# Optimization experiments

Measured on AMD Instinct MI355X. Metric: run time of the kernel, lower is better.

Reference implementation:

```python
import jax, jax.numpy as jnp
import numpy as np

K0 = 16                       # probe slice length (hard-coded in kernel)
TAU = 2.053748910631823       # t-test threshold (|tau| of kernel constant)


def setup_inputs() -> dict:
    key = jax.random.key(0)
    k1, k2, k3 = jax.random.split(key, 3)
    B, DIN, DOUT = 8192, 4096, 4096
    x = jax.random.normal(k1, (B, DIN), dtype=jnp.float32)
    W = jax.random.normal(k2, (DOUT, DIN), dtype=jnp.float32)
    bias = jax.random.normal(k3, (DOUT,), dtype=jnp.float32)
    return {"x": x, "W": W, "bias": bias}


def reference(x, W, bias):
    # --- partial dot over the first K0 columns of K (the probe) ---
    x0 = x[:, :K0]                    # [B, K0]
    w0 = W[:, :K0]                    # [DOUT, K0]
    y1 = x0 @ w0.T                    # [B, DOUT]  sum_k x_k * w_k
    # sum of squared elementwise products: prod_k^2 = x_k^2 * w_k^2
    s2 = (x0 * x0) @ (w0 * w0).T      # [B, DOUT]
    # --- per-(row, column) t-statistic and early-exit decision ---
    tstat = jnp.abs(y1) / jnp.sqrt(s2 / K0)
    passed = tstat < TAU              # True -> column deemed insignificant, zeroed
    # --- full linear (active columns keep full accumulation + bias) ---
    full = x @ W.T + bias[None, :]    # [B, DOUT]
    return jnp.where(passed, 0.0, full)
```

## Files before the change

kernel.cpp:

```cpp
#include <hip/hip_runtime.h>
#include <cstdint>
#include <cstddef>

#define TAU_D 2.053748910631823
#define M_DIM 8192
#define N_DIM 4096
#define K_DIM 4096
#define NIT   32

typedef float f32x4  __attribute__((ext_vector_type(4)));
typedef short bf16x8 __attribute__((ext_vector_type(8)));

typedef __attribute__((address_space(1))) void gvoid_t;
typedef __attribute__((address_space(3))) void lvoid_t;

__device__ __forceinline__ void gload_lds16(const void* g, void* l) {
    __builtin_amdgcn_global_load_lds((const gvoid_t*)g, (lvoid_t*)l, 16, 0, 0);
}

__device__ __forceinline__ unsigned int pack2bf(float lo, float hi) {
    unsigned int ul = __float_as_uint(lo);
    unsigned int uh = __float_as_uint(hi);
    ul = (ul + 0x7FFFu + ((ul >> 16) & 1u)) >> 16;
    uh = (uh + 0x7FFFu + ((uh >> 16) & 1u)) >> 16;
    return ul | (uh << 16);
}

__global__ void cvt_f32_to_bf16(const float4* __restrict__ in,
                                uint2* __restrict__ out, int n4) {
    int i = blockIdx.x * blockDim.x + threadIdx.x;
    const int stride = gridDim.x * blockDim.x;
    for (; i < n4; i += stride) {
        float4 a = in[i];
        uint2 o;
        o.x = pack2bf(a.x, a.y);
        o.y = pack2bf(a.z, a.w);
        out[i] = o;
    }
}

#define BARRIER() do { __builtin_amdgcn_s_barrier(); \
                       __builtin_amdgcn_sched_barrier(0); } while (0)

__global__ __launch_bounds__(512, 2) void gemm_masked8(
    const unsigned short* __restrict__ Ab,
    const unsigned short* __restrict__ Bb,
    const float* __restrict__ X,
    const float* __restrict__ Wt,
    const float* __restrict__ bias,
    float* __restrict__ out)
{
    __shared__ __align__(16) char lds[131072];

    const int tid  = threadIdx.x;
    const int wave = tid >> 6;
    const int lane = tid & 63;
    const int lr = lane & 15;
    const int lq = lane >> 4;
    const int wm = wave >> 2;
    const int wn = wave & 3;

    const int flat = blockIdx.x;
    const int xcd  = flat & 7;
    const int s    = flat >> 3;
    const int rnd  = s >> 5;
    const int jj   = s & 31;
    const int trow = rnd * 16 + ((xcd >> 2) << 3) + (jj >> 2);
    const int tcol = ((xcd & 3) << 2) + (jj & 3);
    const int rowBase = trow * 256;
    const int colBase = tcol * 256;

    f32x4 acc[8][4];
    #pragma unroll
    for (int i = 0; i < 8; ++i)
        #pragma unroll
        for (int n = 0; n < 4; ++n)
            acc[i][n] = (f32x4){0.f, 0.f, 0.f, 0.f};

    const int srow  = tid >> 3;
    const int sslot = (tid & 7) ^ (srow & 7);
    const unsigned short* aSrc =
        Ab + (size_t)(rowBase + srow) * K_DIM + sslot * 8;
    const unsigned short* bSrc =
        Bb + (size_t)(colBase + srow) * K_DIM + sslot * 8;

    const unsigned R0A = 0, R0B = 32768, R1A = 65536, R1B = 98304;

    auto stageA = [&](int kst, unsigned reg) {
        #pragma unroll
        for (int i = 0; i < 4; ++i)
            gload_lds16(aSrc + (size_t)i * 64 * K_DIM + kst * 64,
                        lds + reg + i * 8192 + wave * 1024);
    };
    auto stageB = [&](int kst, unsigned reg) {
        #pragma unroll
        for (int i = 0; i < 4; ++i)
            gload_lds16(bSrc + (size_t)i * 64 * K_DIM + kst * 64,
                        lds + reg + i * 8192 + wave * 1024);
    };

    const unsigned kk0 = (unsigned)((lq) ^ (lr & 7)) * 16;
    const unsigned kk1 = (unsigned)((4 + lq) ^ (lr & 7)) * 16;
    const unsigned rowA = (unsigned)(wm * 128 + lr) * 128;
    const unsigned rowB = (unsigned)(wn * 64 + lr) * 128;

    stageA(0, R0A);
    stageB(0, R0B);
    stageA(1, R1A);
    asm volatile("s_waitcnt vmcnt(4)" ::: "memory");
    BARRIER();

    bf16x8 aF[4][2];
    bf16x8 bF0[2][2];
    bf16x8 bF1[2][2];

    for (int j = 0; j < NIT; ++j) {
        const int ka = 2 * j;
        const int kb = 2 * j + 1;
        const bool stg = (j + 1 < NIT);

        #pragma unroll
        for (int m = 0; m < 4; ++m) {
            aF[m][0] = *(const bf16x8*)(lds + R0A + rowA + m * 2048 + kk0);
            aF[m][1] = *(const bf16x8*)(lds + R0A + rowA + m * 2048 + kk1);
        }
        #pragma unroll
        for (int n = 0; n < 2; ++n) {
            bF0[n][0] = *(const bf16x8*)(lds + R0B + rowB + n * 2048 + kk0);
            bF0[n][1] = *(const bf16x8*)(lds + R0B + rowB + n * 2048 + kk1);
        }
        stageB(kb, R1B);
        BARRIER();
        __builtin_amdgcn_s_setprio(1);
        #pragma unroll
        for (int m = 0; m < 4; ++m)
            #pragma unroll
            for (int n = 0; n < 2; ++n)
                #pragma unroll
                for (int ks = 0; ks < 2; ++ks)
                    acc[m][n] = __builtin_amdgcn_mfma_f32_16x16x32_bf16(
                        aF[m][ks], bF0[n][ks], acc[m][n], 0, 0, 0);
        __builtin_amdgcn_s_setprio(0);
        BARRIER();

        #pragma unroll
        for (int n = 0; n < 2; ++n) {
            bF1[n][0] = *(const bf16x8*)(lds + R0B + rowB + (2 + n) * 2048 + kk0);
            bF1[n][1] = *(const bf16x8*)(lds + R0B + rowB + (2 + n) * 2048 + kk1);
        }
        BARRIER();
        __builtin_amdgcn_s_setprio(1);
        #pragma unroll
        for (int m = 0; m < 4; ++m)
            #pragma unroll
            for (int n = 0; n < 2; ++n)
                #pragma unroll
                for (int ks = 0; ks < 2; ++ks)
                    acc[m][2 + n] = __builtin_amdgcn_mfma_f32_16x16x32_bf16(
                        aF[m][ks], bF1[n][ks], acc[m][2 + n], 0, 0, 0);
        __builtin_amdgcn_s_setprio(0);
        BARRIER();

        #pragma unroll
        for (int m = 0; m < 4; ++m) {
            aF[m][0] = *(const bf16x8*)(lds + R0A + rowA + (4 + m) * 2048 + kk0);
            aF[m][1] = *(const bf16x8*)(lds + R0A + rowA + (4 + m) * 2048 + kk1);
        }
        BARRIER();
        __builtin_amdgcn_s_setprio(1);
        #pragma unroll
        for (int m = 0; m < 4; ++m)
            #pragma unroll
            for (int n = 0; n < 2; ++n)
                #pragma unroll
                for (int ks = 0; ks < 2; ++ks)
                    acc[4 + m][2 + n] = __builtin_amdgcn_mfma_f32_16x16x32_bf16(
                        aF[m][ks], bF1[n][ks], acc[4 + m][2 + n], 0, 0, 0);
        __builtin_amdgcn_s_setprio(0);
        BARRIER();

        if (stg) stageA(ka + 2, R0A);
        BARRIER();
        __builtin_amdgcn_s_setprio(1);
        #pragma unroll
        for (int m = 0; m < 4; ++m)
            #pragma unroll
            for (int n = 0; n < 2; ++n)
                #pragma unroll
                for (int ks = 0; ks < 2; ++ks)
                    acc[4 + m][n] = __builtin_amdgcn_mfma_f32_16x16x32_bf16(
                        aF[m][ks], bF0[n][ks], acc[4 + m][n], 0, 0, 0);
        __builtin_amdgcn_s_setprio(0);
        if (stg) {
            asm volatile("s_waitcnt vmcnt(4)" ::: "memory");
        } else {
            asm volatile("s_waitcnt vmcnt(0)" ::: "memory");
        }
        BARRIER();

        #pragma unroll
        for (int m = 0; m < 4; ++m) {
            aF[m][0] = *(const bf16x8*)(lds + R1A + rowA + m * 2048 + kk0);
            aF[m][1] = *(const bf16x8*)(lds + R1A + rowA + m * 2048 + kk1);
        }
        #pragma unroll
        for (int n = 0; n < 2; ++n) {
            bF0[n][0] = *(const bf16x8*)(lds + R1B + rowB + n * 2048 + kk0);
            bF0[n][1] = *(const bf16x8*)(lds + R1B + rowB + n * 2048 + kk1);
        }
        if (stg) stageB(ka + 2, R0B);
        BARRIER();
        __builtin_amdgcn_s_setprio(1);
        #pragma unroll
        for (int m = 0; m < 4; ++m)
            #pragma unroll
            for (int n = 0; n < 2; ++n)
                #pragma unroll
                for (int ks = 0; ks < 2; ++ks)
                    acc[m][n] = __builtin_amdgcn_mfma_f32_16x16x32_bf16(
                        aF[m][ks], bF0[n][ks], acc[m][n], 0, 0, 0);
        __builtin_amdgcn_s_setprio(0);
        BARRIER();

        #pragma unroll
        for (int n = 0; n < 2; ++n) {
            bF1[n][0] = *(const bf16x8*)(lds + R1B + rowB + (2 + n) * 2048 + kk0);
            bF1[n][1] = *(const bf16x8*)(lds + R1B + rowB + (2 + n) * 2048 + kk1);
        }
        BARRIER();
        __builtin_amdgcn_s_setprio(1);
        #pragma unroll
        for (int m = 0; m < 4; ++m)
            #pragma unroll
            for (int n = 0; n < 2; ++n)
                #pragma unroll
                for (int ks = 0; ks < 2; ++ks)
                    acc[m][2 + n] = __builtin_amdgcn_mfma_f32_16x16x32_bf16(
                        aF[m][ks], bF1[n][ks], acc[m][2 + n], 0, 0, 0);
        __builtin_amdgcn_s_setprio(0);
        BARRIER();

        #pragma unroll
        for (int m = 0; m < 4; ++m) {
            aF[m][0] = *(const bf16x8*)(lds + R1A + rowA + (4 + m) * 2048 + kk0);
            aF[m][1] = *(const bf16x8*)(lds + R1A + rowA + (4 + m) * 2048 + kk1);
        }
        BARRIER();
        __builtin_amdgcn_s_setprio(1);
        #pragma unroll
        for (int m = 0; m < 4; ++m)
            #pragma unroll
            for (int n = 0; n < 2; ++n)
                #pragma unroll
                for (int ks = 0; ks < 2; ++ks)
                    acc[4 + m][2 + n] = __builtin_amdgcn_mfma_f32_16x16x32_bf16(
                        aF[m][ks], bF1[n][ks], acc[4 + m][2 + n], 0, 0, 0);
        __builtin_amdgcn_s_setprio(0);
        BARRIER();

        if (stg) stageA(kb + 2, R1A);
        BARRIER();
        __builtin_amdgcn_s_setprio(1);
        #pragma unroll
        for (int m = 0; m < 4; ++m)
            #pragma unroll
            for (int n = 0; n < 2; ++n)
                #pragma unroll
                for (int ks = 0; ks < 2; ++ks)
                    acc[4 + m][n] = __builtin_amdgcn_mfma_f32_16x16x32_bf16(
                        aF[m][ks], bF0[n][ks], acc[4 + m][n], 0, 0, 0);
        __builtin_amdgcn_s_setprio(0);
        asm volatile("s_waitcnt vmcnt(4)" ::: "memory");
        BARRIER();
    }

    __syncthreads();
    float* x0s = (float*)(lds);
    float* w0s = (float*)(lds + 16384);
    #pragma unroll
    for (int i = 0; i < 2; ++i) {
        int idx = tid + i * 512;
        int r = idx >> 2, qq = (idx & 3) << 2;
        *(f32x4*)(x0s + r * 16 + qq) =
            *(const f32x4*)(X + (size_t)(rowBase + r) * K_DIM + qq);
        *(f32x4*)(w0s + r * 16 + qq) =
            *(const f32x4*)(Wt + (size_t)(colBase + r) * K_DIM + qq);
    }
    __syncthreads();

    const float TAU32 = (float)TAU_D;

    #pragma unroll
    for (int np = 0; np < 4; np += 2) {
        float wv[2][16];
        float bv[2];
        #pragma unroll
        for (int e = 0; e < 2; ++e) {
            const int c = wn * 64 + (np + e) * 16 + lr;
            #pragma unroll
            for (int q = 0; q < 4; ++q)
                *(f32x4*)&wv[e][q * 4] = *(const f32x4*)(w0s + c * 16 + q * 4);
            bv[e] = bias[colBase + c];
        }
        #pragma unroll
        for (int mi = 0; mi < 8; ++mi) {
            #pragma unroll
            for (int jr = 0; jr < 4; ++jr) {
                const int rw = wm * 128 + mi * 16 + lq * 4 + jr;
                float xv[16];
                #pragma unroll
                for (int q = 0; q < 4; ++q)
                    *(f32x4*)&xv[q * 4] = *(const f32x4*)(x0s + rw * 16 + q * 4);
                const size_t orow = (size_t)(rowBase + rw) * N_DIM + colBase;
                #pragma unroll
                for (int e = 0; e < 2; ++e) {
                    const int n = np + e;
                    float y1 = 0.f, s2 = 0.f;
                    #pragma unroll
                    for (int k = 0; k < 16; ++k) {
                        float xk = xv[k], wk = wv[e][k];
                        float xx = xk * xk, ww = wk * wk;
                        y1 = fmaf(xk, wk, y1);
                        s2 = fmaf(xx, ww, s2);
                    }
                    float t = fabsf(y1) / sqrtf(s2 * 0.0625f);
                    float v = (t < TAU32) ? 0.0f : (acc[mi][n][jr] + bv[e]);
                    out[orow + wn * 64 + n * 16 + lr] = v;
                }
            }
        }
    }
}

__global__ __launch_bounds__(256, 2) void gemm_masked_fb(
    const float* __restrict__ X, const float* __restrict__ Wt,
    const float* __restrict__ bias, float* __restrict__ out)
{
    __shared__ __align__(16) unsigned short As[128 * 32];
    __shared__ __align__(16) unsigned short Bs[128 * 32];

    const int tid  = threadIdx.x;
    const int wave = tid >> 6;
    const int lane = tid & 63;
    const int rowBase = blockIdx.y * 128;
    const int colBase = blockIdx.x * 128;
    const int wr = wave >> 1;
    const int wc = wave & 1;
    const int lr = lane & 15;
    const int lq = lane >> 4;

    f32x4 acc[4][4];
    #pragma unroll
    for (int m = 0; m < 4; ++m)
        #pragma unroll
        for (int n = 0; n < 4; ++n)
            acc[m][n] = (f32x4){0.f, 0.f, 0.f, 0.f};

    const int srow = tid >> 2;
    const int scol = (tid & 3) * 8;
    const float* afp = X  + (size_t)(rowBase + srow) * K_DIM + scol;
    const float* bfp = Wt + (size_t)(colBase + srow) * K_DIM + scol;

    for (int kt = 0; kt < K_DIM; kt += 32) {
        #pragma unroll
        for (int issue = 0; issue < 2; ++issue) {
            const float* sa = afp + (size_t)issue * 64 * K_DIM;
            const float* sb = bfp + (size_t)issue * 64 * K_DIM;
            float4 a0 = *(const float4*)(sa);
            float4 a1 = *(const float4*)(sa + 4);
            float4 b0 = *(const float4*)(sb);
            float4 b1 = *(const float4*)(sb + 4);
            uint4 pa, pb;
            pa.x = pack2bf(a0.x, a0.y); pa.y = pack2bf(a0.z, a0.w);
            pa.z = pack2bf(a1.x, a1.y); pa.w = pack2bf(a1.z, a1.w);
            pb.x = pack2bf(b0.x, b0.y); pb.y = pack2bf(b0.z, b0.w);
            pb.z = pack2bf(b1.x, b1.y); pb.w = pack2bf(b1.z, b1.w);
            *(uint4*)((char*)As + issue * 4096 + tid * 16) = pa;
            *(uint4*)((char*)Bs + issue * 4096 + tid * 16) = pb;
        }
        afp += 32; bfp += 32;
        __syncthreads();

        bf16x8 af[4], bq[4];
        #pragma unroll
        for (int m = 0; m < 4; ++m)
            af[m] = *(const bf16x8*)(As + (wr * 64 + m * 16 + lr) * 32 + lq * 8);
        #pragma unroll
        for (int n = 0; n < 4; ++n)
            bq[n] = *(const bf16x8*)(Bs + (wc * 64 + n * 16 + lr) * 32 + lq * 8);
        #pragma unroll
        for (int m = 0; m < 4; ++m)
            #pragma unroll
            for (int n = 0; n < 4; ++n)
                acc[m][n] = __builtin_amdgcn_mfma_f32_16x16x32_bf16(
                    af[m], bq[n], acc[m][n], 0, 0, 0);
        __syncthreads();
    }

    float* x0s = (float*)As;
    float* w0s = (float*)Bs;
    #pragma unroll
    for (int i = 0; i < 2; ++i) {
        int idx = tid + i * 256;
        int r = idx >> 2, q = (idx & 3) * 4;
        *(float4*)(x0s + r * 16 + q) =
            *(const float4*)(X + (size_t)(rowBase + r) * K_DIM + q);
        *(float4*)(w0s + r * 16 + q) =
            *(const float4*)(Wt + (size_t)(colBase + r) * K_DIM + q);
    }
    __syncthreads();

    const float TAU32 = (float)TAU_D;
    float wv[4][16];
    float bv[4];
    #pragma unroll
    for (int n = 0; n < 4; ++n) {
        int c = wc * 64 + n * 16 + lr;
        #pragma unroll
        for (int q = 0; q < 4; ++q)
            *(f32x4*)&wv[n][q * 4] = *(const f32x4*)(w0s + c * 16 + q * 4);
        bv[n] = bias[colBase + c];
    }

    #pragma unroll
    for (int m = 0; m < 4; ++m) {
        #pragma unroll
        for (int j = 0; j < 4; ++j) {
            const int r = wr * 64 + m * 16 + lq * 4 + j;
            float xv[16];
            #pragma unroll
            for (int q = 0; q < 4; ++q)
                *(f32x4*)&xv[q * 4] = *(const f32x4*)(x0s + r * 16 + q * 4);
            const size_t orow = (size_t)(rowBase + r) * N_DIM + colBase;
            #pragma unroll
            for (int n = 0; n < 4; ++n) {
                float y1 = 0.f, s2 = 0.f;
                #pragma unroll
                for (int k = 0; k < 16; ++k) {
                    float xk = xv[k];
                    float wk = wv[n][k];
                    float xx = xk * xk;
                    float ww = wk * wk;
                    y1 = fmaf(xk, wk, y1);
                    s2 = fmaf(xx, ww, s2);
                }
                float t = fabsf(y1) / sqrtf(s2 * 0.0625f);
                float v = (t < TAU32) ? 0.0f : (acc[m][n][j] + bv[n]);
                out[orow + wc * 64 + n * 16 + lr] = v;
            }
        }
    }
}

extern "C" void kernel_launch(void* const* d_in, const int* in_sizes, int n_in,
                              void* d_out, int out_size, void* d_ws, size_t ws_size,
                              hipStream_t stream) {
    const float* x    = (const float*)d_in[0];
    const float* W    = (const float*)d_in[1];
    const float* bias = (const float*)d_in[2];
    float* out = (float*)d_out;

    const size_t needA = (size_t)M_DIM * K_DIM * 2;
    const size_t needB = (size_t)N_DIM * K_DIM * 2;

    if (ws_size >= needA + needB) {
        unsigned short* xb = (unsigned short*)d_ws;
        unsigned short* wb = (unsigned short*)((char*)d_ws + needA);
        cvt_f32_to_bf16<<<2048, 256, 0, stream>>>(
            (const float4*)x, (uint2*)xb, (M_DIM * K_DIM) / 4);
        cvt_f32_to_bf16<<<2048, 256, 0, stream>>>(
            (const float4*)W, (uint2*)wb, (N_DIM * K_DIM) / 4);
        dim3 grid((M_DIM / 256) * (N_DIM / 256));
        gemm_masked8<<<grid, 512, 0, stream>>>(xb, wb, x, W, bias, out);
    } else {
        dim3 grid(N_DIM / 128, M_DIM / 128);
        gemm_masked_fb<<<grid, 256, 0, stream>>>(x, W, bias, out);
    }
}
```

Before: 325.0 us.

## Split global-to-LDS staging into halves spread across MFMA phases

After: 315.9 us. 2.8% less time.

```diff
diff --git a/kernel.cpp b/kernel.cpp
--- a/kernel.cpp
+++ b/kernel.cpp
@@ -40,7 +40,7 @@
 }
 
 #define BARRIER() do { __builtin_amdgcn_s_barrier(); \
-                       __builtin_amdgcn_sched_barrier(0); } while (0)
+                       asm volatile("" ::: "memory"); } while (0)
 
 __global__ __launch_bounds__(512, 2) void gemm_masked8(
     const unsigned short* __restrict__ Ab,
@@ -86,15 +86,15 @@
 
     const unsigned R0A = 0, R0B = 32768, R1A = 65536, R1B = 98304;
 
-    auto stageA = [&](int kst, unsigned reg) {
-        #pragma unroll
-        for (int i = 0; i < 4; ++i)
+    auto stageHalfA = [&](int kst, unsigned reg, int h) {
+        #pragma unroll
+        for (int i = 2 * h; i < 2 * h + 2; ++i)
             gload_lds16(aSrc + (size_t)i * 64 * K_DIM + kst * 64,
                         lds + reg + i * 8192 + wave * 1024);
     };
-    auto stageB = [&](int kst, unsigned reg) {
-        #pragma unroll
-        for (int i = 0; i < 4; ++i)
+    auto stageHalfB = [&](int kst, unsigned reg, int h) {
+        #pragma unroll
+        for (int i = 2 * h; i < 2 * h + 2; ++i)
             gload_lds16(bSrc + (size_t)i * 64 * K_DIM + kst * 64,
                         lds + reg + i * 8192 + wave * 1024);
     };
@@ -104,9 +104,9 @@
     const unsigned rowA = (unsigned)(wm * 128 + lr) * 128;
     const unsigned rowB = (unsigned)(wn * 64 + lr) * 128;
 
-    stageA(0, R0A);
-    stageB(0, R0B);
-    stageA(1, R1A);
+    stageHalfA(0, R0A, 0); stageHalfA(0, R0A, 1);
+    stageHalfB(0, R0B, 0); stageHalfB(0, R0B, 1);
+    stageHalfB(1, R1B, 0); stageHalfB(1, R1B, 1);
     asm volatile("s_waitcnt vmcnt(4)" ::: "memory");
     BARRIER();
 
@@ -129,7 +129,7 @@
             bF0[n][0] = *(const bf16x8*)(lds + R0B + rowB + n * 2048 + kk0);
             bF0[n][1] = *(const bf16x8*)(lds + R0B + rowB + n * 2048 + kk1);
         }
-        stageB(kb, R1B);
+        stageHalfA(kb, R1A, 0);
         BARRIER();
         __builtin_amdgcn_s_setprio(1);
         #pragma unroll
@@ -148,6 +148,7 @@
             bF1[n][0] = *(const bf16x8*)(lds + R0B + rowB + (2 + n) * 2048 + kk0);
             bF1[n][1] = *(const bf16x8*)(lds + R0B + rowB + (2 + n) * 2048 + kk1);
         }
+        stageHalfA(kb, R1A, 1);
         BARRIER();
         __builtin_amdgcn_s_setprio(1);
         #pragma unroll
@@ -166,6 +167,7 @@
             aF[m][0] = *(const bf16x8*)(lds + R0A + rowA + (4 + m) * 2048 + kk0);
             aF[m][1] = *(const bf16x8*)(lds + R0A + rowA + (4 + m) * 2048 + kk1);
         }
+        if (stg) stageHalfB(ka + 2, R0B, 0);
         BARRIER();
         __builtin_amdgcn_s_setprio(1);
         #pragma unroll
@@ -179,8 +181,7 @@
         __builtin_amdgcn_s_setprio(0);
         BARRIER();
 
-        if (stg) stageA(ka + 2, R0A);
-        BARRIER();
+        if (stg) stageHalfB(ka + 2, R0B, 1);
         __builtin_amdgcn_s_setprio(1);
         #pragma unroll
         for (int m = 0; m < 4; ++m)
@@ -208,7 +209,7 @@
             bF0[n][0] = *(const bf16x8*)(lds + R1B + rowB + n * 2048 + kk0);
             bF0[n][1] = *(const bf16x8*)(lds + R1B + rowB + n * 2048 + kk1);
         }
-        if (stg) stageB(ka + 2, R0B);
+        if (stg) stageHalfA(ka + 2, R0A, 0);
         BARRIER();
         __builtin_amdgcn_s_setprio(1);
         #pragma unroll
@@ -227,6 +228,7 @@
             bF1[n][0] = *(const bf16x8*)(lds + R1B + rowB + (2 + n) * 2048 + kk0);
             bF1[n][1] = *(const bf16x8*)(lds + R1B + rowB + (2 + n) * 2048 + kk1);
         }
+        if (stg) stageHalfA(ka + 2, R0A, 1);
         BARRIER();
         __builtin_amdgcn_s_setprio(1);
         #pragma unroll
@@ -245,6 +247,7 @@
             aF[m][0] = *(const bf16x8*)(lds + R1A + rowA + (4 + m) * 2048 + kk0);
             aF[m][1] = *(const bf16x8*)(lds + R1A + rowA + (4 + m) * 2048 + kk1);
         }
+        if (stg) stageHalfB(kb + 2, R1B, 0);
         BARRIER();
         __builtin_amdgcn_s_setprio(1);
         #pragma unroll
@@ -258,8 +261,7 @@
         __builtin_amdgcn_s_setprio(0);
         BARRIER();
 
-        if (stg) stageA(kb + 2, R1A);
-        BARRIER();
+        if (stg) stageHalfB(kb + 2, R1B, 1);
         __builtin_amdgcn_s_setprio(1);
         #pragma unroll
         for (int m = 0; m < 4; ++m)
@@ -270,7 +272,8 @@
                     acc[4 + m][n] = __builtin_amdgcn_mfma_f32_16x16x32_bf16(
                         aF[m][ks], bF0[n][ks], acc[4 + m][n], 0, 0, 0);
         __builtin_amdgcn_s_setprio(0);
-        asm volatile("s_waitcnt vmcnt(4)" ::: "memory");
+        if (stg)
+            asm volatile("s_waitcnt vmcnt(4)" ::: "memory");
         BARRIER();
     }
 
```
